# Kernel tuning notes

Hardware: AMD Instinct MI355X
Metric: run time of the kernel (lower is better)

The kernel has to match this reference:

```python
import jax, jax.numpy as jnp
import numpy as np

DIM = 96
WIN = (5, 6, 5)          # (wd, wh, ww)
SHAPE = (2, 96, 40, 48, 40)  # B, C, D, H, W


def _rel_pos_index(win):
    """Swin-3D relative position index, [N, N] int, N = wd*wh*ww."""
    wd, wh, ww = win
    coords = np.stack(np.meshgrid(np.arange(wd), np.arange(wh), np.arange(ww), indexing='ij'))
    cf = coords.reshape(3, -1)                       # [3, N]
    rel = (cf[:, :, None] - cf[:, None, :]).transpose(1, 2, 0).astype(np.int64)  # [N,N,3]
    rel[..., 0] += wd - 1
    rel[..., 1] += wh - 1
    rel[..., 2] += ww - 1
    rel[..., 0] *= (2 * wh - 1) * (2 * ww - 1)
    rel[..., 1] *= (2 * ww - 1)
    return rel.sum(-1)                               # [N, N]


def _ln(x, g, b):
    m = x.mean(-1, keepdims=True)
    v = x.var(-1, keepdims=True)
    return (x - m) * jax.lax.rsqrt(v + 1e-5) * g + b


def _win_partition(x, win):
    # x: [B, D, H, W, C] -> [B*nW, wd*wh*ww, C]
    B, D, H, W, C = x.shape
    wd, wh, ww = win
    x = x.reshape(B, D // wd, wd, H // wh, wh, W // ww, ww, C)
    x = x.transpose(0, 1, 3, 5, 2, 4, 6, 7)
    return x.reshape(-1, wd * wh * ww, C)


def _win_reverse(xw, win, B, D, H, W):
    wd, wh, ww = win
    C = xw.shape[-1]
    x = xw.reshape(B, D // wd, H // wh, W // ww, wd, wh, ww, C)
    x = x.transpose(0, 1, 4, 2, 5, 3, 6, 7)
    return x.reshape(B, D, H, W, C)


def setup_inputs() -> dict:
    key = jax.random.key(0)
    ks = jax.random.split(key, 16)
    B, C, D, H, W = SHAPE
    hid = 4 * C
    n_bias = (2 * WIN[0] - 1) * (2 * WIN[1] - 1) * (2 * WIN[2] - 1)
    f32 = jnp.float32
    return {
        'I_m': jax.random.normal(ks[0], (B, C, D, H, W), f32),
        'I_f': jax.random.normal(ks[1], (B, C, D, H, W), f32),
        'ln1q_g': jnp.ones((C,), f32), 'ln1q_b': jnp.zeros((C,), f32),
        'ln1kv_g': jnp.ones((C,), f32), 'ln1kv_b': jnp.zeros((C,), f32),
        'wq': jax.random.normal(ks[2], (C, C), f32) * 0.02,
        'bq': jnp.zeros((C,), f32),
        'wkv': jax.random.normal(ks[3], (C, 2 * C), f32) * 0.02,
        'bkv': jnp.zeros((2 * C,), f32),
        'wproj': jax.random.normal(ks[4], (C, C), f32) * 0.02,
        'bproj': jnp.zeros((C,), f32),
        'rel_bias': jax.random.normal(ks[5], (n_bias, 1), f32) * 0.02,
        'ln2_g': jnp.ones((C,), f32), 'ln2_b': jnp.zeros((C,), f32),
        'mlp_w1': jax.random.normal(ks[6], (C, hid), f32) * 0.02,
        'mlp_b1': jnp.zeros((hid,), f32),
        'mlp_w2': jax.random.normal(ks[7], (hid, C), f32) * 0.02,
        'mlp_b2': jnp.zeros((C,), f32),
        'conv_w': jax.random.normal(ks[8], (3, C, 3, 3, 3), f32) * 1e-5,  # RegistrationHead Normal(0,1e-5)
        'conv_b': jnp.zeros((3,), f32),
    }


def reference(I_m, I_f, ln1q_g, ln1q_b, ln1kv_g, ln1kv_b, wq, bq, wkv, bkv,
              wproj, bproj, rel_bias, ln2_g, ln2_b, mlp_w1, mlp_b1, mlp_w2,
              mlp_b2, conv_w, conv_b):
    B, C, D, H, W = I_m.shape
    N = WIN[0] * WIN[1] * WIN[2]
    idx = jnp.asarray(_rel_pos_index(WIN))           # [N, N] constant

    # channels-last tokens
    x = I_m.transpose(0, 2, 3, 4, 1)                 # [B, D, H, W, C]
    y = I_f.transpose(0, 2, 3, 4, 1)
    shortcut = x

    xw = _win_partition(_ln(x, ln1q_g, ln1q_b), WIN)   # [BnW, N, C]
    yw = _win_partition(_ln(y, ln1kv_g, ln1kv_b), WIN)

    q = xw @ wq + bq                                  # [BnW, N, C]
    kv = yw @ wkv + bkv
    k, v = kv[..., :C], kv[..., C:]

    scale = C ** -0.5                                 # num_heads = 1
    bias = rel_bias[idx].squeeze(-1)                  # [N, N]
    attn = jnp.einsum('wnc,wmc->wnm', q, k) * scale + bias
    attn = jax.nn.softmax(attn, axis=-1)
    out = jnp.einsum('wnm,wmc->wnc', attn, v) @ wproj + bproj

    x = shortcut + _win_reverse(out, WIN, B, D, H, W)
    h = _ln(x, ln2_g, ln2_b)
    x = x + (jax.nn.gelu(h @ mlp_w1 + mlp_b1) @ mlp_w2 + mlp_b2)

    feat = x.transpose(0, 4, 1, 2, 3)                 # [B, C, D, H, W]
    flow = jax.lax.conv_general_dilated(
        feat, conv_w, window_strides=(1, 1, 1), padding=[(1, 1)] * 3,
        dimension_numbers=('NCDHW', 'OIDHW', 'NCDHW'))
    return flow + conv_b[None, :, None, None, None]
```

## Files before the change

### kernel.cpp

```cpp
#include <hip/hip_runtime.h>
#include <math.h>


static constexpr int NTOK = 153600;
static constexpr float SCALE = 0.10206207261596575f;

typedef __bf16 bf16_t;
typedef __bf16 bf16x8 __attribute__((ext_vector_type(8)));
typedef float f32x4 __attribute__((ext_vector_type(4)));

__device__ __forceinline__ int tok_index(int b, int d, int h, int w) {
    int d0 = d / 5, wd = d % 5;
    int h0 = h / 6, wh = h % 6;
    int w0 = w / 5, ww = w % 5;
    int win = ((b * 8 + d0) * 8 + h0) * 8 + w0;
    return win * 150 + (wd * 6 + wh) * 5 + ww;
}

__device__ __forceinline__ float gelu_f(float u) {
    float u2 = u * u;
    float arg = u * fmaf(0.0713549f, u2, 1.5957691f);
    float e = __expf(arg);
    float r = __builtin_amdgcn_rcpf(e + 1.f);
    return fmaf(-u, r, u);
}

__global__ __launch_bounds__(256) void k_prep_weights(
    const float* __restrict__ wq, const float* __restrict__ wkv,
    const float* __restrict__ w1, const float* __restrict__ w2,
    const float* __restrict__ wproj, const float* __restrict__ relb,
    const float* __restrict__ cw,
    bf16_t* wqT, bf16_t* wkvT, bf16_t* w1T, bf16_t* w2T, bf16_t* wpjT,
    float* bias_mat, float* cwT)
{
    int i = blockIdx.x * 256 + threadIdx.x;
    if (i < 9216)  wqT[i]  = (bf16_t)wq[(i % 96) * 96 + i / 96];
    if (i < 18432) wkvT[i] = (bf16_t)wkv[(i % 96) * 192 + i / 96];
    if (i < 36864) w1T[i]  = (bf16_t)w1[(i % 96) * 384 + i / 96];
    if (i < 36864) w2T[i]  = (bf16_t)w2[(i % 384) * 96 + i / 384];
    if (i < 9216)  wpjT[i] = (bf16_t)wproj[(i % 96) * 96 + i / 96];
    if (i < 25600) {
        int row = i / 160, col = i % 160;
        float v;
        if (col >= 150) v = -1e30f;
        else if (row >= 150) v = 0.f;
        else {
            int wd1 = row / 30, rh1 = row % 30, wh1 = rh1 / 5, ww1 = rh1 % 5;
            int wd2 = col / 30, rh2 = col % 30, wh2 = rh2 / 5, ww2 = rh2 % 5;
            int idx = (wd1 - wd2 + 4) * 99 + (wh1 - wh2 + 5) * 9 + (ww1 - ww2 + 4);
            v = relb[idx];
        }
        bias_mat[i] = v;
    }
    if (i < 7776) {
        int kk = i / 288, rem = i % 288;
        int oc = rem / 96, ci = rem % 96;
        cwT[i] = cw[oc * 2592 + ci * 27 + kk];
    }
}

__global__ __launch_bounds__(256) void k_ln_transpose(
    const float* __restrict__ Im, const float* __restrict__ If,
    const float* __restrict__ g1q, const float* __restrict__ b1q,
    const float* __restrict__ g1k, const float* __restrict__ b1k,
    bf16_t* __restrict__ xln, bf16_t* __restrict__ yln,
    float* __restrict__ x2s)
{
    __shared__ float tile[80 * 97];
    __shared__ float red_s[80][3], red2_s[80][3];
    __shared__ float mean_s[80], rstd_s[80];
    int blk = blockIdx.x;
    int b = blk / (40 * 24);
    int rem = blk % (40 * 24);
    int d = rem / 24, hp = rem % 24;
    int h0 = hp * 2;
    int tid = threadIdx.x;

    for (int pass = 0; pass < 2; ++pass) {
        const float* src = pass ? If : Im;
        const float* gg = pass ? g1k : g1q;
        const float* bb = pass ? b1k : b1q;
        bf16_t* dst = pass ? yln : xln;

        for (int i = tid; i < 1920; i += 256) {
            int c = i / 20, q = i % 20;
            float4 v = *(const float4*)(src + (size_t)(b * 96 + c) * 76800
                                        + d * 1920 + h0 * 40 + q * 4);
            int w0 = q * 4;
            tile[(w0 + 0) * 97 + c] = v.x;
            tile[(w0 + 1) * 97 + c] = v.y;
            tile[(w0 + 2) * 97 + c] = v.z;
            tile[(w0 + 3) * 97 + c] = v.w;
        }
        __syncthreads();
        if (tid < 240) {
            int w6 = tid / 3, j = tid % 3;
            const float* tp = tile + w6 * 97 + j * 32;
            float s = 0.f, s2 = 0.f;
#pragma unroll
            for (int c = 0; c < 32; ++c) { float v = tp[c]; s += v; s2 += v * v; }
            red_s[w6][j] = s;
            red2_s[w6][j] = s2;
        }
        __syncthreads();
        if (tid < 80) {
            float s = red_s[tid][0] + red_s[tid][1] + red_s[tid][2];
            float s2 = red2_s[tid][0] + red2_s[tid][1] + red2_s[tid][2];
            float m = s * (1.f / 96.f);
            float var = s2 * (1.f / 96.f) - m * m;
            mean_s[tid] = m;
            rstd_s[tid] = rsqrtf(var + 1e-5f);
        }
        __syncthreads();
        for (int i = tid; i < 960; i += 256) {
            int w = i / 12, c8 = i % 12;
            int hh = h0 + (w >= 40), ww = w - (w >= 40) * 40;
            int tok = tok_index(b, d, hh, ww);
            float m = mean_s[w], rs = rstd_s[w];
            const float4* ggv = (const float4*)(gg + c8 * 8);
            const float4* bbv = (const float4*)(bb + c8 * 8);
            float4 g0 = ggv[0], g1 = ggv[1];
            float4 b0 = bbv[0], b1v = bbv[1];
            const float* tp = tile + w * 97 + c8 * 8;
            float x0 = tp[0], x1 = tp[1], x2v = tp[2], x3 = tp[3];
            float x4 = tp[4], x5 = tp[5], x6 = tp[6], x7 = tp[7];
            bf16x8 tb;
            tb[0] = (bf16_t)((x0 - m) * rs * g0.x + b0.x);
            tb[1] = (bf16_t)((x1 - m) * rs * g0.y + b0.y);
            tb[2] = (bf16_t)((x2v - m) * rs * g0.z + b0.z);
            tb[3] = (bf16_t)((x3 - m) * rs * g0.w + b0.w);
            tb[4] = (bf16_t)((x4 - m) * rs * g1.x + b1v.x);
            tb[5] = (bf16_t)((x5 - m) * rs * g1.y + b1v.y);
            tb[6] = (bf16_t)((x6 - m) * rs * g1.z + b1v.z);
            tb[7] = (bf16_t)((x7 - m) * rs * g1.w + b1v.w);
            *(bf16x8*)(dst + (size_t)tok * 96 + c8 * 8) = tb;
            if (pass == 0) {
                float* xp = x2s + (size_t)tok * 96 + c8 * 8;
                *(float4*)(xp) = make_float4(x0, x1, x2v, x3);
                *(float4*)(xp + 4) = make_float4(x4, x5, x6, x7);
            }
        }
        __syncthreads();
    }
}

__global__ __launch_bounds__(256) void k_proj_mfma(
    const bf16_t* __restrict__ X, const bf16_t* __restrict__ WT,
    const float* __restrict__ bias, int N,
    bf16_t* __restrict__ outA, bf16_t* __restrict__ vT)
{
    extern __shared__ bf16_t sm[];
    bf16_t* xs  = sm;
    bf16_t* wsh = sm + 64 * 104;
    int tid = threadIdx.x;
    int t0 = blockIdx.x * 64;

    const uint4* xg = (const uint4*)(X + (size_t)t0 * 96);
    uint4* xsv = (uint4*)xs;
    for (int i = tid; i < 768; i += 256) {
        int row = i / 12, c16 = i % 12;
        xsv[row * 13 + c16] = xg[i];
    }
    const uint4* wg = (const uint4*)WT;
    uint4* wsv = (uint4*)wsh;
    for (int i = tid; i < N * 12; i += 256) {
        int row = i / 12, c16 = i % 12;
        wsv[row * 13 + c16] = wg[i];
    }
    __syncthreads();

    int w = tid >> 6, l = tid & 63;
    int lm = l & 15, lk = (l >> 4) * 8;
    int m0 = w * 16;
    bf16x8 a[3];
#pragma unroll
    for (int kk = 0; kk < 3; ++kk)
        a[kk] = *(const bf16x8*)(xs + (m0 + lm) * 104 + kk * 32 + lk);

    int trow[4], twin[4], tm[4];
#pragma unroll
    for (int r = 0; r < 4; ++r) {
        int t = t0 + m0 + (l >> 4) * 4 + r;
        trow[r] = t; twin[r] = t / 150; tm[r] = t - twin[r] * 150;
    }

    int ntiles = N >> 4;
    for (int ti = 0; ti < ntiles; ++ti) {
        int n0 = ti * 16;
        f32x4 c = {0.f, 0.f, 0.f, 0.f};
        const bf16_t* wp = wsh + (size_t)(n0 + lm) * 104 + lk;
        c = __builtin_amdgcn_mfma_f32_16x16x32_bf16(a[0], *(const bf16x8*)(wp), c, 0, 0, 0);
        c = __builtin_amdgcn_mfma_f32_16x16x32_bf16(a[1], *(const bf16x8*)(wp + 32), c, 0, 0, 0);
        c = __builtin_amdgcn_mfma_f32_16x16x32_bf16(a[2], *(const bf16x8*)(wp + 64), c, 0, 0, 0);
        int n = n0 + lm;
        float bs = bias[n];
        if (n < 96) {
#pragma unroll
            for (int r = 0; r < 4; ++r)
                outA[(size_t)trow[r] * 96 + n] = (bf16_t)(c[r] + bs);
        } else {
            int cc = n - 96;
#pragma unroll
            for (int r = 0; r < 4; ++r)
                vT[((size_t)twin[r] * 96 + cc) * 160 + tm[r]] = (bf16_t)(c[r] + bs);
        }
    }
}

__global__ __launch_bounds__(256, 4) void k_attn_mfma(
    const bf16_t* __restrict__ qb, const bf16_t* __restrict__ kb,
    const bf16_t* __restrict__ vT, const bf16_t* __restrict__ wpjT,
    const float* __restrict__ bias_mat, const float* __restrict__ bproj,
    bf16_t* __restrict__ aob)
{
    __shared__ __align__(16) bf16_t pls_all[4 * 16 * 164];
    int tid = threadIdx.x;
    int wv = tid >> 6, l = tid & 63;
    int task = blockIdx.x * 4 + wv;
    int win = task / 10, ti = task - win * 10;
    int lm = l & 15, lq = l >> 4, lk8 = lq * 8;
    size_t wbase = (size_t)win * 150 * 96;
    size_t vbase = (size_t)win * 96 * 160;
    bf16_t* pls = pls_all + wv * 16 * 164;
    int r0 = ti * 16;

    bf16x8 aq[3];
#pragma unroll
    for (int kk = 0; kk < 3; ++kk)
        aq[kk] = *(const bf16x8*)(qb + wbase + (size_t)(r0 + lm) * 96 + kk * 32 + lk8);

    f32x4 s[10];
#pragma unroll
    for (int nt = 0; nt < 10; ++nt) {
        int krow = nt * 16 + lm;
        if (krow > 149) krow = 149;
        f32x4 acc = {0.f, 0.f, 0.f, 0.f};
        const bf16_t* kp = kb + wbase + (size_t)krow * 96 + lk8;
        acc = __builtin_amdgcn_mfma_f32_16x16x32_bf16(aq[0], *(const bf16x8*)(kp), acc, 0, 0, 0);
        acc = __builtin_amdgcn_mfma_f32_16x16x32_bf16(aq[1], *(const bf16x8*)(kp + 32), acc, 0, 0, 0);
        acc = __builtin_amdgcn_mfma_f32_16x16x32_bf16(aq[2], *(const bf16x8*)(kp + 64), acc, 0, 0, 0);
        s[nt] = acc;
    }

#pragma unroll
    for (int r = 0; r < 4; ++r) {
        int grow = r0 + lq * 4 + r;
        float rowmax = -3.0e38f;
#pragma unroll
        for (int nt = 0; nt < 10; ++nt) {
            float bv = bias_mat[grow * 160 + nt * 16 + lm];
            float v = fmaf(s[nt][r], SCALE, bv);
            s[nt][r] = v;
            rowmax = fmaxf(rowmax, v);
        }
        rowmax = fmaxf(rowmax, __shfl_xor(rowmax, 1));
        rowmax = fmaxf(rowmax, __shfl_xor(rowmax, 2));
        rowmax = fmaxf(rowmax, __shfl_xor(rowmax, 4));
        rowmax = fmaxf(rowmax, __shfl_xor(rowmax, 8));
        float ssum = 0.f;
#pragma unroll
        for (int nt = 0; nt < 10; ++nt) {
            float e = __expf(s[nt][r] - rowmax);
            s[nt][r] = e;
            ssum += e;
        }
        ssum += __shfl_xor(ssum, 1);
        ssum += __shfl_xor(ssum, 2);
        ssum += __shfl_xor(ssum, 4);
        ssum += __shfl_xor(ssum, 8);
        float inv = 1.f / ssum;
        int lrow = lq * 4 + r;
#pragma unroll
        for (int nt = 0; nt < 10; ++nt)
            pls[lrow * 164 + nt * 16 + lm] = (bf16_t)(s[nt][r] * inv);
    }

    f32x4 o[6];
#pragma unroll
    for (int ct = 0; ct < 6; ++ct) o[ct] = (f32x4){0.f, 0.f, 0.f, 0.f};
#pragma unroll
    for (int kf = 0; kf < 5; ++kf) {
        bf16x8 ap = *(const bf16x8*)(pls + lm * 164 + kf * 32 + lk8);
#pragma unroll
        for (int ct = 0; ct < 6; ++ct) {
            const bf16_t* vp = vT + vbase + (size_t)(ct * 16 + lm) * 160 + kf * 32 + lk8;
            o[ct] = __builtin_amdgcn_mfma_f32_16x16x32_bf16(ap, *(const bf16x8*)(vp), o[ct], 0, 0, 0);
        }
    }

#pragma unroll
    for (int ct = 0; ct < 6; ++ct)
#pragma unroll
        for (int r = 0; r < 4; ++r)
            pls[(lq * 4 + r) * 104 + ct * 16 + lm] = (bf16_t)o[ct][r];

    bf16x8 ao[3];
#pragma unroll
    for (int kk = 0; kk < 3; ++kk)
        ao[kk] = *(const bf16x8*)(pls + lm * 104 + kk * 32 + lk8);
    f32x4 pj[6];
#pragma unroll
    for (int ct = 0; ct < 6; ++ct) {
        f32x4 acc = {0.f, 0.f, 0.f, 0.f};
        const bf16_t* wp = wpjT + (size_t)(ct * 16 + lm) * 96 + lk8;
        acc = __builtin_amdgcn_mfma_f32_16x16x32_bf16(ao[0], *(const bf16x8*)(wp), acc, 0, 0, 0);
        acc = __builtin_amdgcn_mfma_f32_16x16x32_bf16(ao[1], *(const bf16x8*)(wp + 32), acc, 0, 0, 0);
        acc = __builtin_amdgcn_mfma_f32_16x16x32_bf16(ao[2], *(const bf16x8*)(wp + 64), acc, 0, 0, 0);
        pj[ct] = acc;
    }
#pragma unroll
    for (int r = 0; r < 4; ++r) {
        int gr = r0 + lq * 4 + r;
        if (gr < 150) {
            size_t t = (size_t)win * 150 + gr;
#pragma unroll
            for (int ct = 0; ct < 6; ++ct) {
                int c = ct * 16 + lm;
                aob[t * 96 + c] = (bf16_t)(pj[ct][r] + bproj[c]);
            }
        }
    }
}

__global__ __launch_bounds__(256, 3) void k_mlp_mfma(
    const float* __restrict__ x2,
    const bf16_t* __restrict__ aob,
    const float* __restrict__ g2, const float* __restrict__ b2,
    const bf16_t* __restrict__ w1T, const float* __restrict__ b1,
    const bf16_t* __restrict__ w2T, const float* __restrict__ b2v,
    bf16_t* __restrict__ xc)
{
    __shared__ __align__(16) bf16_t xs[128 * 104];
    __shared__ __align__(16) bf16_t wsm[96 * 104];

    int tid = threadIdx.x;
    int t0 = blockIdx.x * 128;

    {
        int t = tid >> 1, p = tid & 1;
        float xr[48];
        const float4* xg = (const float4*)(x2 + (size_t)(t0 + t) * 96 + p * 48);
        const bf16x8* ag = (const bf16x8*)(aob + (size_t)(t0 + t) * 96 + p * 48);
#pragma unroll
        for (int j4 = 0; j4 < 12; ++j4) {
            float4 v = xg[j4];
            xr[j4 * 4 + 0] = v.x; xr[j4 * 4 + 1] = v.y;
            xr[j4 * 4 + 2] = v.z; xr[j4 * 4 + 3] = v.w;
        }
#pragma unroll
        for (int j8 = 0; j8 < 6; ++j8) {
            bf16x8 av = ag[j8];
#pragma unroll
            for (int e = 0; e < 8; ++e)
                xr[j8 * 8 + e] += (float)av[e];
        }
        float s = 0.f, s2 = 0.f;
#pragma unroll
        for (int j = 0; j < 48; ++j) { s += xr[j]; s2 += xr[j] * xr[j]; }
        s += __shfl_xor(s, 1);
        s2 += __shfl_xor(s2, 1);
        float m = s * (1.f / 96.f);
        float var = s2 * (1.f / 96.f) - m * m;
        float rstd = rsqrtf(var + 1e-5f);

        const float4* gg = (const float4*)(g2 + p * 48);
        const float4* bb = (const float4*)(b2 + p * 48);
        bf16_t tmp[48];
#pragma unroll
        for (int j4 = 0; j4 < 12; ++j4) {
            float4 g = gg[j4], bv = bb[j4];
            tmp[j4 * 4 + 0] = (bf16_t)((xr[j4 * 4 + 0] - m) * rstd * g.x + bv.x);
            tmp[j4 * 4 + 1] = (bf16_t)((xr[j4 * 4 + 1] - m) * rstd * g.y + bv.y);
            tmp[j4 * 4 + 2] = (bf16_t)((xr[j4 * 4 + 2] - m) * rstd * g.z + bv.z);
            tmp[j4 * 4 + 3] = (bf16_t)((xr[j4 * 4 + 3] - m) * rstd * g.w + bv.w);
        }
        uint4* dst = (uint4*)(xs + t * 104 + p * 48);
        const uint4* src = (const uint4*)tmp;
#pragma unroll
        for (int j = 0; j < 6; ++j) dst[j] = src[j];
    }

    int w = tid >> 6, l = tid & 63;
    int lm = l & 15, lq = l >> 4, lk = lq * 8;
    int m0 = w * 32;
    bf16_t* hw = xs + w * 32 * 104;

    bf16x8 a[2][3];
#pragma unroll
    for (int mt = 0; mt < 2; ++mt)
#pragma unroll
        for (int kk = 0; kk < 3; ++kk)
            a[mt][kk] = *(const bf16x8*)(xs + (m0 + mt * 16 + lm) * 104 + kk * 32 + lk);

    f32x4 acc2[2][6];
#pragma unroll
    for (int mt = 0; mt < 2; ++mt)
#pragma unroll
        for (int i = 0; i < 6; ++i) acc2[mt][i] = (f32x4){0.f, 0.f, 0.f, 0.f};

    auto stage_w = [&](const bf16_t* src, int srcStride) {
        uint4* wv = (uint4*)wsm;
        for (int i = tid; i < 1152; i += 256) {
            int row = i / 12, c = i - row * 12;
            wv[row * 13 + c] = *(const uint4*)(src + (size_t)row * srcStride + c * 8);
        }
    };

#pragma unroll
    for (int cc = 0; cc < 4; ++cc) {
        stage_w(w1T + (size_t)cc * 96 * 96, 96);
        __syncthreads();
#pragma unroll
        for (int ti = 0; ti < 6; ++ti) {
            int n = cc * 96 + ti * 16 + lm;
            const bf16_t* wp = wsm + (size_t)(ti * 16 + lm) * 104 + lk;
            bf16x8 w0 = *(const bf16x8*)(wp);
            bf16x8 w1v = *(const bf16x8*)(wp + 32);
            bf16x8 w2v = *(const bf16x8*)(wp + 64);
            float bs = b1[n];
#pragma unroll
            for (int mt = 0; mt < 2; ++mt) {
                f32x4 c1 = {0.f, 0.f, 0.f, 0.f};
                c1 = __builtin_amdgcn_mfma_f32_16x16x32_bf16(a[mt][0], w0, c1, 0, 0, 0);
                c1 = __builtin_amdgcn_mfma_f32_16x16x32_bf16(a[mt][1], w1v, c1, 0, 0, 0);
                c1 = __builtin_amdgcn_mfma_f32_16x16x32_bf16(a[mt][2], w2v, c1, 0, 0, 0);
#pragma unroll
                for (int r = 0; r < 4; ++r)
                    hw[(mt * 16 + lq * 4 + r) * 104 + ti * 16 + lm] =
                        (bf16_t)gelu_f(c1[r] + bs);
            }
        }
        __syncthreads();

        stage_w(w2T + (size_t)cc * 96, 384);
        __syncthreads();
        bf16x8 ha[2][3];
#pragma unroll
        for (int mt = 0; mt < 2; ++mt)
#pragma unroll
            for (int kk = 0; kk < 3; ++kk)
                ha[mt][kk] = *(const bf16x8*)(hw + (mt * 16 + lm) * 104 + kk * 32 + lk);
#pragma unroll
        for (int ti = 0; ti < 6; ++ti) {
            const bf16_t* wp = wsm + (size_t)(ti * 16 + lm) * 104 + lk;
            bf16x8 v0 = *(const bf16x8*)(wp);
            bf16x8 v1 = *(const bf16x8*)(wp + 32);
            bf16x8 v2 = *(const bf16x8*)(wp + 64);
#pragma unroll
            for (int mt = 0; mt < 2; ++mt) {
                acc2[mt][ti] = __builtin_amdgcn_mfma_f32_16x16x32_bf16(ha[mt][0], v0, acc2[mt][ti], 0, 0, 0);
                acc2[mt][ti] = __builtin_amdgcn_mfma_f32_16x16x32_bf16(ha[mt][1], v1, acc2[mt][ti], 0, 0, 0);
                acc2[mt][ti] = __builtin_amdgcn_mfma_f32_16x16x32_bf16(ha[mt][2], v2, acc2[mt][ti], 0, 0, 0);
            }
        }
        if (cc < 3) __syncthreads();
    }

#pragma unroll
    for (int mt = 0; mt < 2; ++mt) {
        int srow[4];
#pragma unroll
        for (int r = 0; r < 4; ++r) {
            int t = t0 + m0 + mt * 16 + lq * 4 + r;
            int win = t / 150, nn = t - win * 150;
            int b = win >> 9, d0 = (win >> 6) & 7, h0 = (win >> 3) & 7, w0 = win & 7;
            int wd = nn / 30, rem = nn % 30, wh = rem / 5, ww = rem % 5;
            srow[r] = ((b * 40 + d0 * 5 + wd) * 48 + h0 * 6 + wh) * 40 + w0 * 5 + ww;
        }
#pragma unroll
        for (int ti = 0; ti < 6; ++ti) {
            int n = ti * 16 + lm;
            float bs = b2v[n];
#pragma unroll
            for (int r = 0; r < 4; ++r) {
                int t = t0 + m0 + mt * 16 + lq * 4 + r;
                size_t o = (size_t)t * 96 + n;
                float base = x2[o] + (float)aob[o];
                xc[(size_t)srow[r] * 96 + n] = (bf16_t)(base + acc2[mt][ti][r] + bs);
            }
        }
    }
}

__global__ __launch_bounds__(256) void k_conv(
    const bf16_t* __restrict__ xc, const float* __restrict__ cwT,
    const float* __restrict__ cb, float* __restrict__ out)
{
    __shared__ float wl[7776];
    int tid = threadIdx.x;
    for (int i = tid; i < 7776; i += 256) wl[i] = cwT[i];
    __syncthreads();

    int gid = blockIdx.x * 256 + tid;
    int s = gid >> 2, p = gid & 3;
    int b = s / 76800, r = s % 76800;
    int d = r / 1920, h = (r / 40) % 48, w = r % 40;
    float a0 = 0.f, a1 = 0.f, a2 = 0.f;

    for (int dd = 0; dd < 3; ++dd) {
        int d2 = d + dd - 1;
        if ((unsigned)d2 >= 40u) continue;
        for (int hh = 0; hh < 3; ++hh) {
            int h2 = h + hh - 1;
            if ((unsigned)h2 >= 48u) continue;
            for (int ww = 0; ww < 3; ++ww) {
                int w2 = w + ww - 1;
                if ((unsigned)w2 >= 40u) continue;
                int kk = (dd * 3 + hh) * 3 + ww;
                const bf16x8* xp = (const bf16x8*)
                    (xc + ((size_t)((b * 40 + d2) * 48 + h2) * 40 + w2) * 96 + p * 24);
                const float* wk = wl + kk * 288 + p * 24;
#pragma unroll
                for (int c8 = 0; c8 < 3; ++c8) {
                    bf16x8 xv = xp[c8];
                    float x0 = (float)xv[0], x1 = (float)xv[1];
                    float x2v = (float)xv[2], x3 = (float)xv[3];
                    float x4 = (float)xv[4], x5 = (float)xv[5];
                    float x6 = (float)xv[6], x7 = (float)xv[7];
                    float4 wa0 = *(const float4*)(wk + c8 * 8);
                    float4 wb0 = *(const float4*)(wk + c8 * 8 + 4);
                    float4 wa1 = *(const float4*)(wk + 96 + c8 * 8);
                    float4 wb1 = *(const float4*)(wk + 96 + c8 * 8 + 4);
                    float4 wa2 = *(const float4*)(wk + 192 + c8 * 8);
                    float4 wb2 = *(const float4*)(wk + 192 + c8 * 8 + 4);
                    a0 += x0 * wa0.x + x1 * wa0.y + x2v * wa0.z + x3 * wa0.w
                        + x4 * wb0.x + x5 * wb0.y + x6 * wb0.z + x7 * wb0.w;
                    a1 += x0 * wa1.x + x1 * wa1.y + x2v * wa1.z + x3 * wa1.w
                        + x4 * wb1.x + x5 * wb1.y + x6 * wb1.z + x7 * wb1.w;
                    a2 += x0 * wa2.x + x1 * wa2.y + x2v * wa2.z + x3 * wa2.w
                        + x4 * wb2.x + x5 * wb2.y + x6 * wb2.z + x7 * wb2.w;
                }
            }
        }
    }
    a0 += __shfl_xor(a0, 1); a0 += __shfl_xor(a0, 2);
    a1 += __shfl_xor(a1, 1); a1 += __shfl_xor(a1, 2);
    a2 += __shfl_xor(a2, 1); a2 += __shfl_xor(a2, 2);
    float av = (p == 0) ? a0 : ((p == 1) ? a1 : a2);
    if (p < 3)
        out[(size_t)(b * 3 + p) * 76800 + r] = av + cb[p];
}

extern "C" void kernel_launch(void* const* d_in, const int* in_sizes, int n_in,
                              void* d_out, int out_size, void* d_ws, size_t ws_size,
                              hipStream_t stream)
{
    (void)in_sizes; (void)n_in; (void)out_size;

    const float* Im  = (const float*)d_in[0];
    const float* If  = (const float*)d_in[1];
    const float* g1q = (const float*)d_in[2];
    const float* b1q = (const float*)d_in[3];
    const float* g1k = (const float*)d_in[4];
    const float* b1k = (const float*)d_in[5];
    const float* wq  = (const float*)d_in[6];
    const float* bq  = (const float*)d_in[7];
    const float* wkv = (const float*)d_in[8];
    const float* bkv = (const float*)d_in[9];
    const float* wpj = (const float*)d_in[10];
    const float* bpj = (const float*)d_in[11];
    const float* rb  = (const float*)d_in[12];
    const float* g2  = (const float*)d_in[13];
    const float* b2  = (const float*)d_in[14];
    const float* w1  = (const float*)d_in[15];
    const float* b1  = (const float*)d_in[16];
    const float* w2  = (const float*)d_in[17];
    const float* b2v = (const float*)d_in[18];
    const float* cw  = (const float*)d_in[19];
    const float* cb  = (const float*)d_in[20];
    float* out = (float*)d_out;

    size_t U = (size_t)NTOK * 96;
    if (ws_size < 4 * U * sizeof(float)) return;
    float* ws = (float*)d_ws;
    bf16_t* xlnb = (bf16_t*)ws;
    bf16_t* ylnb = (bf16_t*)(ws + U / 2);
    bf16_t* qb   = (bf16_t*)(ws + U);
    bf16_t* kb   = (bf16_t*)(ws + 3 * U / 2);
    bf16_t* vT   = (bf16_t*)(ws + 2 * U);
    float*  wtail = ws + 2 * U + (1024 * 96 * 160) / 2;
    bf16_t* wqT  = (bf16_t*)wtail;
    bf16_t* wkvT = wqT + 9216;
    bf16_t* w1T  = wkvT + 18432;
    bf16_t* w2T  = w1T + 36864;
    bf16_t* wpjT = w2T + 36864;
    float*  bias_mat = (float*)(wpjT + 9216 + 2);
    float*  cwT  = bias_mat + 25600;
    float*  x2f  = ws + 3 * U;
    bf16_t* aob  = (bf16_t*)ws;
    bf16_t* xc   = (bf16_t*)(ws + U / 2);

    k_prep_weights<<<144, 256, 0, stream>>>(wq, wkv, w1, w2, wpj, rb, cw,
                                            wqT, wkvT, w1T, w2T, wpjT,
                                            bias_mat, cwT);
    k_ln_transpose<<<1920, 256, 0, stream>>>(Im, If, g1q, b1q, g1k, b1k,
                                             xlnb, ylnb, x2f);
    size_t shm_q  = (size_t)(64 * 104 + 96 * 104) * sizeof(bf16_t);
    size_t shm_kv = (size_t)(64 * 104 + 192 * 104) * sizeof(bf16_t);
    k_proj_mfma<<<2400, 256, shm_q, stream>>>(xlnb, wqT, bq, 96, qb, nullptr);
    k_proj_mfma<<<2400, 256, shm_kv, stream>>>(ylnb, wkvT, bkv, 192, kb, vT);
    k_attn_mfma<<<2560, 256, 0, stream>>>(qb, kb, vT, wpjT, bias_mat, bpj, aob);
    k_mlp_mfma<<<1200, 256, 0, stream>>>(x2f, aob, g2, b2, w1T, b1, w2T, b2v, xc);
    k_conv<<<2400, 256, 0, stream>>>(xc, cwT, cb, out);
}
```

Measured before the change: 482.7 us.

## Rewrite 3D conv as implicit GEMM using bf16 MFMA with padded output channels

The final 3x3x3 convolution (96 to 3 channels) now runs on MFMA 16x16x32 bf16 instructions. Output channels are zero-padded to 16 and the weights are stored in bf16. Out-of-bounds taps read from a zero buffer instead of branching. The aim is to replace per-thread scalar FMA work and the LDS weight staging with matrix instructions, at the cost of wasting 13 of the 16 output columns and rounding the conv weights to bf16.

```diff
diff --git a/kernel.cpp b/kernel.cpp
--- a/kernel.cpp
+++ b/kernel.cpp
@@ -31,7 +31,7 @@
     const float* __restrict__ wproj, const float* __restrict__ relb,
     const float* __restrict__ cw,
     bf16_t* wqT, bf16_t* wkvT, bf16_t* w1T, bf16_t* w2T, bf16_t* wpjT,
-    float* bias_mat, float* cwT)
+    float* bias_mat, bf16_t* wcvT, bf16_t* zpad)
 {
     int i = blockIdx.x * 256 + threadIdx.x;
     if (i < 9216)  wqT[i]  = (bf16_t)wq[(i % 96) * 96 + i / 96];
@@ -52,11 +52,12 @@
         }
         bias_mat[i] = v;
     }
-    if (i < 7776) {
-        int kk = i / 288, rem = i % 288;
-        int oc = rem / 96, ci = rem % 96;
-        cwT[i] = cw[oc * 2592 + ci * 27 + kk];
-    }
+    if (i < 41472) {
+        int kk = i / 1536, rem2 = i % 1536;
+        int oc = rem2 / 96, ci = rem2 % 96;
+        wcvT[i] = (bf16_t)(oc < 3 ? cw[oc * 2592 + ci * 27 + kk] : 0.f);
+    }
+    if (i < 96) zpad[i] = (bf16_t)0.f;
 }
 
 __global__ __launch_bounds__(256) void k_ln_transpose(
@@ -483,62 +484,65 @@
 }
 
 __global__ __launch_bounds__(256) void k_conv(
-    const bf16_t* __restrict__ xc, const float* __restrict__ cwT,
+    const bf16_t* __restrict__ xc, const bf16_t* __restrict__ wcvT,
+    const bf16_t* __restrict__ zpad,
     const float* __restrict__ cb, float* __restrict__ out)
 {
-    __shared__ float wl[7776];
     int tid = threadIdx.x;
-    for (int i = tid; i < 7776; i += 256) wl[i] = cwT[i];
-    __syncthreads();
-
-    int gid = blockIdx.x * 256 + tid;
-    int s = gid >> 2, p = gid & 3;
-    int b = s / 76800, r = s % 76800;
-    int d = r / 1920, h = (r / 40) % 48, w = r % 40;
-    float a0 = 0.f, a1 = 0.f, a2 = 0.f;
-
+    int wv = tid >> 6, l = tid & 63;
+    int lm = l & 15, lq = l >> 4, lk8 = lq * 8;
+    int p0 = blockIdx.x * 64 + wv * 16;
+    int p = p0 + lm;
+    int b = p / 76800, rr = p % 76800;
+    int d = rr / 1920, h = (rr / 40) % 48, w = rr % 40;
+
+    f32x4 c0 = {0.f, 0.f, 0.f, 0.f};
+    f32x4 c1v = {0.f, 0.f, 0.f, 0.f};
+
+#pragma unroll
     for (int dd = 0; dd < 3; ++dd) {
         int d2 = d + dd - 1;
-        if ((unsigned)d2 >= 40u) continue;
+        bool okd = (unsigned)d2 < 40u;
+#pragma unroll
         for (int hh = 0; hh < 3; ++hh) {
             int h2 = h + hh - 1;
-            if ((unsigned)h2 >= 48u) continue;
+            bool okh = (unsigned)h2 < 48u;
+#pragma unroll
             for (int ww = 0; ww < 3; ++ww) {
                 int w2 = w + ww - 1;
-                if ((unsigned)w2 >= 40u) continue;
+                bool ok = okd && okh && ((unsigned)w2 < 40u);
                 int kk = (dd * 3 + hh) * 3 + ww;
-                const bf16x8* xp = (const bf16x8*)
-                    (xc + ((size_t)((b * 40 + d2) * 48 + h2) * 40 + w2) * 96 + p * 24);
-                const float* wk = wl + kk * 288 + p * 24;
-#pragma unroll
-                for (int c8 = 0; c8 < 3; ++c8) {
-                    bf16x8 xv = xp[c8];
-                    float x0 = (float)xv[0], x1 = (float)xv[1];
-                    float x2v = (float)xv[2], x3 = (float)xv[3];
-                    float x4 = (float)xv[4], x5 = (float)xv[5];
-                    float x6 = (float)xv[6], x7 = (float)xv[7];
-                    float4 wa0 = *(const float4*)(wk + c8 * 8);
-                    float4 wb0 = *(const float4*)(wk + c8 * 8 + 4);
-                    float4 wa1 = *(const float4*)(wk + 96 + c8 * 8);
-                    float4 wb1 = *(const float4*)(wk + 96 + c8 * 8 + 4);
-                    float4 wa2 = *(const float4*)(wk + 192 + c8 * 8);
-                    float4 wb2 = *(const float4*)(wk + 192 + c8 * 8 + 4);
-                    a0 += x0 * wa0.x + x1 * wa0.y + x2v * wa0.z + x3 * wa0.w
-                        + x4 * wb0.x + x5 * wb0.y + x6 * wb0.z + x7 * wb0.w;
-                    a1 += x0 * wa1.x + x1 * wa1.y + x2v * wa1.z + x3 * wa1.w
-                        + x4 * wb1.x + x5 * wb1.y + x6 * wb1.z + x7 * wb1.w;
-                    a2 += x0 * wa2.x + x1 * wa2.y + x2v * wa2.z + x3 * wa2.w
-                        + x4 * wb2.x + x5 * wb2.y + x6 * wb2.z + x7 * wb2.w;
+                int src = ((b * 40 + d2) * 48 + h2) * 40 + w2;
+                const bf16_t* pa = ok ? (xc + (size_t)src * 96) : zpad;
+                const bf16_t* pb = wcvT + kk * 1536 + lm * 96;
+                if (kk & 1) {
+                    c1v = __builtin_amdgcn_mfma_f32_16x16x32_bf16(
+                        *(const bf16x8*)(pa + lk8), *(const bf16x8*)(pb + lk8), c1v, 0, 0, 0);
+                    c1v = __builtin_amdgcn_mfma_f32_16x16x32_bf16(
+                        *(const bf16x8*)(pa + 32 + lk8), *(const bf16x8*)(pb + 32 + lk8), c1v, 0, 0, 0);
+                    c1v = __builtin_amdgcn_mfma_f32_16x16x32_bf16(
+                        *(const bf16x8*)(pa + 64 + lk8), *(const bf16x8*)(pb + 64 + lk8), c1v, 0, 0, 0);
+                } else {
+                    c0 = __builtin_amdgcn_mfma_f32_16x16x32_bf16(
+                        *(const bf16x8*)(pa + lk8), *(const bf16x8*)(pb + lk8), c0, 0, 0, 0);
+                    c0 = __builtin_amdgcn_mfma_f32_16x16x32_bf16(
+                        *(const bf16x8*)(pa + 32 + lk8), *(const bf16x8*)(pb + 32 + lk8), c0, 0, 0, 0);
+                    c0 = __builtin_amdgcn_mfma_f32_16x16x32_bf16(
+                        *(const bf16x8*)(pa + 64 + lk8), *(const bf16x8*)(pb + 64 + lk8), c0, 0, 0, 0);
                 }
             }
         }
     }
-    a0 += __shfl_xor(a0, 1); a0 += __shfl_xor(a0, 2);
-    a1 += __shfl_xor(a1, 1); a1 += __shfl_xor(a1, 2);
-    a2 += __shfl_xor(a2, 1); a2 += __shfl_xor(a2, 2);
-    float av = (p == 0) ? a0 : ((p == 1) ? a1 : a2);
-    if (p < 3)
-        out[(size_t)(b * 3 + p) * 76800 + r] = av + cb[p];
+
+    if (lm < 3) {
+        float bsv = cb[lm];
+#pragma unroll
+        for (int r = 0; r < 4; ++r) {
+            int pt = p0 + lq * 4 + r;
+            int bb2 = pt / 76800, rp = pt % 76800;
+            out[(size_t)(bb2 * 3 + lm) * 76800 + rp] = c0[r] + c1v[r] + bsv;
+        }
+    }
 }
 
 extern "C" void kernel_launch(void* const* d_in, const int* in_sizes, int n_in,
@@ -585,14 +589,15 @@
     bf16_t* w2T  = w1T + 36864;
     bf16_t* wpjT = w2T + 36864;
     float*  bias_mat = (float*)(wpjT + 9216 + 2);
-    float*  cwT  = bias_mat + 25600;
+    bf16_t* wcvT = (bf16_t*)(bias_mat + 25600);
+    bf16_t* zpad = wcvT + 41472;
     float*  x2f  = ws + 3 * U;
     bf16_t* aob  = (bf16_t*)ws;
     bf16_t* xc   = (bf16_t*)(ws + U / 2);
 
-    k_prep_weights<<<144, 256, 0, stream>>>(wq, wkv, w1, w2, wpj, rb, cw,
+    k_prep_weights<<<162, 256, 0, stream>>>(wq, wkv, w1, w2, wpj, rb, cw,
                                             wqT, wkvT, w1T, w2T, wpjT,
-                                            bias_mat, cwT);
+                                            bias_mat, wcvT, zpad);
     k_ln_transpose<<<1920, 256, 0, stream>>>(Im, If, g1q, b1q, g1k, b1k,
                                              xlnb, ylnb, x2f);
     size_t shm_q  = (size_t)(64 * 104 + 96 * 104) * sizeof(bf16_t);
@@ -601,5 +606,5 @@
     k_proj_mfma<<<2400, 256, shm_kv, stream>>>(ylnb, wkvT, bkv, 192, kb, vT);
     k_attn_mfma<<<2560, 256, 0, stream>>>(qb, kb, vT, wpjT, bias_mat, bpj, aob);
     k_mlp_mfma<<<1200, 256, 0, stream>>>(x2f, aob, g2, b2, w1T, b1, w2T, b2v, xc);
-    k_conv<<<2400, 256, 0, stream>>>(xc, cwT, cb, out);
-}
+    k_conv<<<2400, 256, 0, stream>>>(xc, wcvT, zpad, cb, out);
+}
```

Result: slower. 507.9 us (+5.2%).

## Split conv channel quarters across waves and read weights as wave-uniform scalars

Applied to the files above, without the earlier changes.

The conv kernel no longer has four adjacent lanes split the channels of one voxel. Each wave now owns a 24-channel quarter, and its 64 lanes cover 64 voxels. The weight index is wave-uniform, so weights can come through scalar loads straight from global memory, and the 31KB LDS weight copy is removed. Partial sums are combined through a small shared buffer with one barrier, replacing the lane shuffles. This cuts LDS use and weight traffic but makes lane loads 192 bytes apart, which coalesces worse. Halo branches also now diverge per voxel inside a wave.

```diff
diff --git a/kernel.cpp b/kernel.cpp
--- a/kernel.cpp
+++ b/kernel.cpp
@@ -486,16 +486,15 @@
     const bf16_t* __restrict__ xc, const float* __restrict__ cwT,
     const float* __restrict__ cb, float* __restrict__ out)
 {
-    __shared__ float wl[7776];
+    __shared__ float red[4][64][3];
     int tid = threadIdx.x;
-    for (int i = tid; i < 7776; i += 256) wl[i] = cwT[i];
-    __syncthreads();
-
-    int gid = blockIdx.x * 256 + tid;
-    int s = gid >> 2, p = gid & 3;
+    int wv = __builtin_amdgcn_readfirstlane(tid >> 6);
+    int l = tid & 63;
+    int s = blockIdx.x * 64 + l;
     int b = s / 76800, r = s % 76800;
     int d = r / 1920, h = (r / 40) % 48, w = r % 40;
     float a0 = 0.f, a1 = 0.f, a2 = 0.f;
+    const float* wq0 = cwT + wv * 24;
 
     for (int dd = 0; dd < 3; ++dd) {
         int d2 = d + dd - 1;
@@ -508,8 +507,8 @@
                 if ((unsigned)w2 >= 40u) continue;
                 int kk = (dd * 3 + hh) * 3 + ww;
                 const bf16x8* xp = (const bf16x8*)
-                    (xc + ((size_t)((b * 40 + d2) * 48 + h2) * 40 + w2) * 96 + p * 24);
-                const float* wk = wl + kk * 288 + p * 24;
+                    (xc + ((size_t)((b * 40 + d2) * 48 + h2) * 40 + w2) * 96 + wv * 24);
+                const float* wk = wq0 + kk * 288;
 #pragma unroll
                 for (int c8 = 0; c8 < 3; ++c8) {
                     bf16x8 xv = xp[c8];
@@ -517,28 +516,31 @@
                     float x2v = (float)xv[2], x3 = (float)xv[3];
                     float x4 = (float)xv[4], x5 = (float)xv[5];
                     float x6 = (float)xv[6], x7 = (float)xv[7];
-                    float4 wa0 = *(const float4*)(wk + c8 * 8);
-                    float4 wb0 = *(const float4*)(wk + c8 * 8 + 4);
-                    float4 wa1 = *(const float4*)(wk + 96 + c8 * 8);
-                    float4 wb1 = *(const float4*)(wk + 96 + c8 * 8 + 4);
-                    float4 wa2 = *(const float4*)(wk + 192 + c8 * 8);
-                    float4 wb2 = *(const float4*)(wk + 192 + c8 * 8 + 4);
-                    a0 += x0 * wa0.x + x1 * wa0.y + x2v * wa0.z + x3 * wa0.w
-                        + x4 * wb0.x + x5 * wb0.y + x6 * wb0.z + x7 * wb0.w;
-                    a1 += x0 * wa1.x + x1 * wa1.y + x2v * wa1.z + x3 * wa1.w
-                        + x4 * wb1.x + x5 * wb1.y + x6 * wb1.z + x7 * wb1.w;
-                    a2 += x0 * wa2.x + x1 * wa2.y + x2v * wa2.z + x3 * wa2.w
-                        + x4 * wb2.x + x5 * wb2.y + x6 * wb2.z + x7 * wb2.w;
+                    const float* w0p = wk + c8 * 8;
+                    const float* w1p = wk + 96 + c8 * 8;
+                    const float* w2p = wk + 192 + c8 * 8;
+                    a0 += x0 * w0p[0] + x1 * w0p[1] + x2v * w0p[2] + x3 * w0p[3]
+                        + x4 * w0p[4] + x5 * w0p[5] + x6 * w0p[6] + x7 * w0p[7];
+                    a1 += x0 * w1p[0] + x1 * w1p[1] + x2v * w1p[2] + x3 * w1p[3]
+                        + x4 * w1p[4] + x5 * w1p[5] + x6 * w1p[6] + x7 * w1p[7];
+                    a2 += x0 * w2p[0] + x1 * w2p[1] + x2v * w2p[2] + x3 * w2p[3]
+                        + x4 * w2p[4] + x5 * w2p[5] + x6 * w2p[6] + x7 * w2p[7];
                 }
             }
         }
     }
-    a0 += __shfl_xor(a0, 1); a0 += __shfl_xor(a0, 2);
-    a1 += __shfl_xor(a1, 1); a1 += __shfl_xor(a1, 2);
-    a2 += __shfl_xor(a2, 1); a2 += __shfl_xor(a2, 2);
-    float av = (p == 0) ? a0 : ((p == 1) ? a1 : a2);
-    if (p < 3)
-        out[(size_t)(b * 3 + p) * 76800 + r] = av + cb[p];
+    red[wv][l][0] = a0;
+    red[wv][l][1] = a1;
+    red[wv][l][2] = a2;
+    __syncthreads();
+    if (tid < 192) {
+        int pt = tid / 3, oc = tid - pt * 3;
+        float v = red[0][pt][oc] + red[1][pt][oc]
+                + red[2][pt][oc] + red[3][pt][oc] + cb[oc];
+        int s2 = blockIdx.x * 64 + pt;
+        int b2 = s2 / 76800, r2 = s2 % 76800;
+        out[(size_t)(b2 * 3 + oc) * 76800 + r2] = v;
+    }
 }
 
 extern "C" void kernel_launch(void* const* d_in, const int* in_sizes, int n_in,
```

New measurement: 485.6 us, median of 2. No clear change (+0.6%).
